# Kernel tuning notes

Hardware: AMD Instinct MI355X
Metric: run time of the kernel (lower is better)

Reference implementation:

```python
import jax, jax.numpy as jnp
import numpy as np

N, D, DFF, E, K = 2048, 1024, 4096, 8, 2  # tokens, d_model, d_ff, num_expert, top_k


def setup_inputs() -> dict:
    key = jax.random.key(0)
    ks = jax.random.split(key, 5)
    s = 0.02  # init scale
    return {
        "moe_inp": jax.random.normal(ks[0], (N, D), jnp.float32),
        "Wg": jax.random.normal(ks[1], (D, E), jnp.float32) * s,   # gate linear
        "bg": jnp.zeros((E,), jnp.float32),
        "W1": jax.random.normal(ks[2], (E, D, DFF), jnp.float32) * s,  # htoh4 per expert
        "b1": jnp.zeros((E, DFF), jnp.float32),
        "W2": jax.random.normal(ks[3], (E, DFF, D), jnp.float32) * s,  # h4toh per expert
        "b2": jnp.zeros((E, D), jnp.float32),
    }


def reference(moe_inp, Wg, bg, W1, b1, W2, b2):
    # --- NaiveGate: top-k experts per token, softmax over selected logits ---
    logits = moe_inp @ Wg + bg                      # [N, E]
    top_val, top_idx = jax.lax.top_k(logits, K)     # [N, K]
    score = jax.nn.softmax(top_val, axis=-1)        # [N, K]

    # Dense combine weights c[n, e] = sum_j score[n, j] * 1{top_idx[n, j] == e}.
    # This is the mathematically exact equivalent of scatter -> grouped expert
    # GEMM -> gather -> score-weighted combine in fmoe.
    comb = jnp.einsum(
        "nke,nk->ne", jax.nn.one_hot(top_idx, E, dtype=moe_inp.dtype), score
    )                                               # [N, E]

    # --- per-expert FFN: relu(x W1 + b1) W2 + b2, masked-combined by comb ---
    h = jax.nn.relu(jnp.einsum("nd,edh->enh", moe_inp, W1) + b1[:, None, :])  # [E, N, DFF]
    out = jnp.einsum("enh,ehd,ne->nd", h, W2, comb) + comb @ b2               # [N, D]
    return out
```

## Files before the change

### kernel.cpp

```cpp
#include <hip/hip_runtime.h>
#include <hip/hip_bf16.h>
#include <cstdint>
#include <cstddef>

#define NTOKS  2048
#define DMODEL 1024
#define DFFN   4096
#define NEXP   8
#define TS256  24
#define TS128  40

typedef __attribute__((ext_vector_type(8))) short short8;
typedef __attribute__((ext_vector_type(4))) float f32x4;
typedef __attribute__((ext_vector_type(4))) unsigned short u16x4;
typedef __attribute__((ext_vector_type(8))) unsigned short u16x8;

static constexpr size_t alignup(size_t x) { return (x + 255) & ~(size_t)255; }
static constexpr size_t OFF_XB   = 0;
static constexpr size_t OFF_CNT  = alignup(OFF_XB + (size_t)(NTOKS + 1) * DMODEL * 2);
static constexpr size_t OFF_OFFS = OFF_CNT + 256;
static constexpr size_t OFF_TOKE = OFF_OFFS + 256;
static constexpr size_t OFF_TOKT = OFF_TOKE + (size_t)NTOKS * 2 * 4;
static constexpr size_t OFF_TOKS = OFF_TOKT + (size_t)NTOKS * 2 * 4;
static constexpr size_t OFF_TI   = alignup(OFF_TOKS + (size_t)NTOKS * 2 * 4);
static constexpr size_t OFF_TI2  = OFF_TI + 256;
static constexpr size_t OFF_CAP  = alignup(OFF_TI2 + TS128 * 8);
static constexpr size_t OFF_H    = alignup(OFF_CAP + (size_t)NEXP * NTOKS * 4);
static constexpr size_t OFF_Y    = alignup(OFF_H + (size_t)(NTOKS * 2 + 256) * DFFN * 2);
static constexpr size_t OFF_WB   = alignup(OFF_Y + (size_t)2 * NTOKS * 2 * DMODEL * 4);

__device__ inline unsigned short f2bf(float f) {
  __hip_bfloat16 h = __float2bfloat16(f);
  return __builtin_bit_cast(unsigned short, h);
}

__device__ inline void gload16(const void* g, void* l) {
  __builtin_amdgcn_global_load_lds((const __attribute__((address_space(1))) unsigned int*)g,
                                   (__attribute__((address_space(3))) unsigned int*)l, 16, 0, 0);
}

__global__ __launch_bounds__(256) void k_convert(const float* __restrict__ x,
                                                 unsigned short* __restrict__ xb,
                                                 int* __restrict__ cnt) {
  if (blockIdx.x == 0 && threadIdx.x < NEXP) cnt[threadIdx.x] = 0;
  size_t base = ((size_t)blockIdx.x * 256 + threadIdx.x) * 8;
  const size_t total = (size_t)(NTOKS + 1) * DMODEL;
  if (base >= total) return;
  u16x8 o;
  if (base < (size_t)NTOKS * DMODEL) {
    f32x4 a = *(const f32x4*)(x + base);
    f32x4 b = *(const f32x4*)(x + base + 4);
#pragma unroll
    for (int j = 0; j < 4; ++j) { o[j] = f2bf(a[j]); o[4 + j] = f2bf(b[j]); }
  } else {
#pragma unroll
    for (int j = 0; j < 8; ++j) o[j] = 0;
  }
  *(u16x8*)(xb + base) = o;
}

template <int R, int C>
__global__ __launch_bounds__(256) void k_transconv(const float* __restrict__ W,
                                                   unsigned short* __restrict__ WT) {
  __shared__ unsigned short T[64][66];
  const int e = blockIdx.z;
  const int c0 = blockIdx.x * 64, r0 = blockIdx.y * 64;
  const float* Wp = W + (size_t)e * R * C;
  unsigned short* Tp = WT + (size_t)e * R * C;
  const int tid = threadIdx.x;
  const int rr = tid >> 4, cc = (tid & 15) << 2;
#pragma unroll
  for (int i = 0; i < 4; ++i) {
    int r = rr + (i << 4);
    f32x4 v = *(const f32x4*)(Wp + (size_t)(r0 + r) * C + c0 + cc);
    T[r][cc]     = f2bf(v[0]);
    T[r][cc + 1] = f2bf(v[1]);
    T[r][cc + 2] = f2bf(v[2]);
    T[r][cc + 3] = f2bf(v[3]);
  }
  __syncthreads();
  const int c = tid >> 2, kc = (tid & 3) << 4;
  u16x8 o0, o1;
#pragma unroll
  for (int i = 0; i < 8; ++i) { o0[i] = T[kc + i][c]; o1[i] = T[kc + 8 + i][c]; }
  unsigned short* dst = Tp + (size_t)(c0 + c) * R + r0 + kc;
  *(u16x8*)(dst) = o0;
  *(u16x8*)(dst + 8) = o1;
}

__global__ __launch_bounds__(256) void k_gate(const float* __restrict__ x,
                                              const float* __restrict__ Wg,
                                              const float* __restrict__ bg,
                                              int* __restrict__ cnt,
                                              int* __restrict__ tok_e,
                                              int* __restrict__ tok_t,
                                              float* __restrict__ tok_s,
                                              int* __restrict__ cap) {
  const int w = threadIdx.x >> 6, lane = threadIdx.x & 63;
  const int n = blockIdx.x * 4 + w;
  float acc[8];
#pragma unroll
  for (int e = 0; e < 8; ++e) acc[e] = 0.f;
  const float* xr = x + (size_t)n * DMODEL;
#pragma unroll 4
  for (int it = 0; it < DMODEL / 64; ++it) {
    int d = it * 64 + lane;
    float xv = xr[d];
    f32x4 w0 = *(const f32x4*)(Wg + d * 8);
    f32x4 w1 = *(const f32x4*)(Wg + d * 8 + 4);
#pragma unroll
    for (int j = 0; j < 4; ++j) { acc[j] += xv * w0[j]; acc[4 + j] += xv * w1[j]; }
  }
#pragma unroll
  for (int e = 0; e < 8; ++e)
#pragma unroll
    for (int off = 32; off; off >>= 1) acc[e] += __shfl_xor(acc[e], off, 64);
  if (lane == 0) {
    float l[8];
#pragma unroll
    for (int e = 0; e < 8; ++e) l[e] = acc[e] + bg[e];
    int i0 = 0; float v0 = l[0];
#pragma unroll
    for (int e = 1; e < 8; ++e) if (l[e] > v0) { v0 = l[e]; i0 = e; }
    int i1 = (i0 == 0) ? 1 : 0; float v1 = l[i1];
#pragma unroll
    for (int e = 0; e < 8; ++e) if (e != i0 && l[e] > v1) { v1 = l[e]; i1 = e; }
    float t = expf(v1 - v0);
    float inv = 1.f / (1.f + t);
    float s0 = inv, s1 = t * inv;
    int t0 = atomicAdd(&cnt[i0], 1);
    int t1 = atomicAdd(&cnt[i1], 1);
    cap[i0 * NTOKS + t0] = n;
    cap[i1 * NTOKS + t1] = n;
    tok_e[2 * n] = i0; tok_e[2 * n + 1] = i1;
    tok_t[2 * n] = t0; tok_t[2 * n + 1] = t1;
    tok_s[2 * n] = s0; tok_s[2 * n + 1] = s1;
  }
}

__global__ void k_scan(const int* __restrict__ cnt, int* __restrict__ offs,
                       int2* __restrict__ ti256, int2* __restrict__ ti128) {
  if (threadIdx.x == 0) {
    int s = 0;
#pragma unroll
    for (int e = 0; e < NEXP; ++e) { offs[e] = s; s += cnt[e]; }
    int a = 0;
    for (int e = 0; e < NEXP; ++e)
      for (int t = 0; t * 256 < cnt[e]; ++t) { ti256[a] = make_int2(e, t * 256); ++a; }
    for (; a < TS256; ++a) ti256[a] = make_int2(-1, 0);
    int b = 0;
    for (int e = 0; e < NEXP; ++e)
      for (int t = 0; t * 128 < cnt[e]; ++t) { ti128[b] = make_int2(e, t * 128); ++b; }
    for (; b < TS128; ++b) ti128[b] = make_int2(-1, 0);
  }
}

__global__ __launch_bounds__(512, 2) void k_gemm8(const unsigned short* __restrict__ Asrc,
                                                  const unsigned short* __restrict__ Bsrc,
                                                  const float* __restrict__ bias,
                                                  const int* __restrict__ cnt,
                                                  const int* __restrict__ offs,
                                                  const int2* __restrict__ tinfo,
                                                  const int* __restrict__ cap,
                                                  unsigned short* __restrict__ hout) {
  constexpr int KTOT = DMODEL, NTOT = DFFN;
  constexpr int NTILES = KTOT / 64;
  constexpr int NI = NTILES / 2;
  const int2 ti = tinfo[blockIdx.y];
  if (ti.x < 0) return;
  const int e = ti.x, t0 = ti.y;
  const int c = cnt[e];
  const int base = offs[e] + t0;
  const int n0 = blockIdx.x * 256;

  const int tid = threadIdx.x, w = tid >> 6, lane = tid & 63;
  const int l15 = lane & 15, lq = lane >> 4;
  const int wr = w >> 2, wc = w & 3;

  __shared__ unsigned short As[2][256 * 64];
  __shared__ unsigned short Bs[2][256 * 64];

  const int rl = tid >> 3;
  const int sw = ((tid & 7) ^ (rl & 7)) << 3;
  const unsigned short* aptr[4];
#pragma unroll
  for (int r = 0; r < 4; ++r) {
    int row = r * 64 + rl;
    size_t gr = (size_t)((t0 + row < c) ? cap[e * NTOKS + t0 + row] : NTOKS);
    aptr[r] = Asrc + gr * (size_t)KTOT + sw;
  }
  const unsigned short* Be = Bsrc + (size_t)e * ((size_t)KTOT * NTOT);
  const unsigned short* bptr[4];
#pragma unroll
  for (int r = 0; r < 4; ++r)
    bptr[r] = Be + (size_t)(n0 + r * 64 + rl) * KTOT + sw;

  auto stage_tile = [&](int tl) {
    const int b = tl & 1;
    const int k0 = tl << 6;
#pragma unroll
    for (int r = 0; r < 4; ++r)
      gload16(aptr[r] + k0, &As[b][(r * 64 + (w << 3)) << 6]);
#pragma unroll
    for (int r = 0; r < 4; ++r)
      gload16(bptr[r] + k0, &Bs[b][(r * 64 + (w << 3)) << 6]);
  };

  f32x4 acc[8][4] = {};
  short8 alo[4], ahi[4];
  const int sw0 = (lq ^ (l15 & 7)) << 3;

  stage_tile(0);
  asm volatile("s_waitcnt vmcnt(0)" ::: "memory");
  __builtin_amdgcn_s_barrier();
  asm volatile("" ::: "memory");

#define PHASE(BUF, MH, NH)                                                          \
  {                                                                                 \
    if ((NH) == 0) {                                                                \
      _Pragma("unroll")                                                             \
      for (int mm = 0; mm < 4; ++mm) {                                              \
        const unsigned short* ab =                                                  \
            &As[BUF][((wr * 128 + (MH) * 64 + mm * 16 + l15) << 6)];                \
        alo[mm] = *(const short8*)&ab[sw0];                                         \
        ahi[mm] = *(const short8*)&ab[sw0 ^ 32];                                    \
      }                                                                             \
    }                                                                               \
    short8 blo[2], bhi[2];                                                          \
    _Pragma("unroll")                                                               \
    for (int nn = 0; nn < 2; ++nn) {                                                \
      const unsigned short* bb =                                                    \
          &Bs[BUF][((wc * 64 + (NH) * 32 + nn * 16 + l15) << 6)];                   \
      blo[nn] = *(const short8*)&bb[sw0];                                           \
      bhi[nn] = *(const short8*)&bb[sw0 ^ 32];                                      \
    }                                                                               \
    asm volatile("" ::: "memory");                                                  \
    __builtin_amdgcn_s_setprio(1);                                                  \
    _Pragma("unroll")                                                               \
    for (int mm = 0; mm < 4; ++mm)                                                  \
      _Pragma("unroll")                                                             \
      for (int nn = 0; nn < 2; ++nn) {                                              \
        acc[(MH) * 4 + mm][(NH) * 2 + nn] =                                         \
            __builtin_amdgcn_mfma_f32_16x16x32_bf16(                                \
                alo[mm], blo[nn], acc[(MH) * 4 + mm][(NH) * 2 + nn], 0, 0, 0);      \
        acc[(MH) * 4 + mm][(NH) * 2 + nn] =                                         \
            __builtin_amdgcn_mfma_f32_16x16x32_bf16(                                \
                ahi[mm], bhi[nn], acc[(MH) * 4 + mm][(NH) * 2 + nn], 0, 0, 0);      \
      }                                                                             \
    __builtin_amdgcn_s_setprio(0);                                                  \
  }
#define FENCE_BAR                                                                   \
  asm volatile("" ::: "memory");                                                    \
  __builtin_amdgcn_s_barrier();                                                     \
  asm volatile("" ::: "memory");
#define DRAIN_BAR                                                                   \
  asm volatile("s_waitcnt vmcnt(0)" ::: "memory");                                  \
  __builtin_amdgcn_s_barrier();                                                     \
  asm volatile("" ::: "memory");

  for (int i = 0; i < NI; ++i) {
    const int t2 = 2 * i;
    stage_tile(t2 + 1);
    PHASE(0, 0, 0) FENCE_BAR
    PHASE(0, 0, 1) FENCE_BAR
    PHASE(0, 1, 0) FENCE_BAR
    PHASE(0, 1, 1) DRAIN_BAR
    if (i + 1 < NI) stage_tile(t2 + 2);
    PHASE(1, 0, 0) FENCE_BAR
    PHASE(1, 0, 1) FENCE_BAR
    PHASE(1, 1, 0) FENCE_BAR
    PHASE(1, 1, 1) DRAIN_BAR
  }
#undef PHASE
#undef FENCE_BAR
#undef DRAIN_BAR

  const float* be = bias + (size_t)e * NTOT;
#pragma unroll
  for (int m = 0; m < 8; ++m) {
#pragma unroll
    for (int q2 = 0; q2 < 4; ++q2) {
      int row = wr * 128 + m * 16 + lq * 4 + q2;
      if (t0 + row < c) {
        unsigned short* hr = hout + (size_t)(base + row) * NTOT;
#pragma unroll
        for (int nn = 0; nn < 4; ++nn) {
          int col = n0 + wc * 64 + nn * 16 + l15;
          float v = acc[m][nn][q2] + be[col];
          v = v > 0.f ? v : 0.f;
          hr[col] = f2bf(v);
        }
      }
    }
  }
}

template <int KTOT, int NTOT, int BN, bool FIRST, int KSPLIT>
__global__ __launch_bounds__(256) void k_gemm(const unsigned short* __restrict__ Asrc,
                                              const unsigned short* __restrict__ Bsrc,
                                              const float* __restrict__ bias,
                                              const int* __restrict__ cnt,
                                              const int* __restrict__ offs,
                                              const int2* __restrict__ tinfo,
                                              const int* __restrict__ cap,
                                              unsigned short* __restrict__ hout,
                                              float* __restrict__ yout) {
  const int2 ti = tinfo[blockIdx.y];
  if (ti.x < 0) return;
  const int e = ti.x, t0 = ti.y;
  const int c = cnt[e];
  const int base = offs[e] + t0;
  const int n0 = blockIdx.x * BN;
  constexpr int KCH = KTOT / KSPLIT;
  constexpr int NT = KCH / 32;
  const int kb = blockIdx.z * KCH;

  const int tid = threadIdx.x, w = tid >> 6, lane = tid & 63;
  const int l15 = lane & 15, lq = lane >> 4;
  constexpr int MR = 4;
  constexpr int NR = BN / 32;
  constexpr int BR = BN / 64;
  const int wr = w >> 1, wc = w & 1;

  __shared__ unsigned short As[2][128 * 32];
  __shared__ unsigned short Bs[2][BN * 32];

  const int rl = tid >> 2;
  const int sw = (((tid & 3) ^ (rl & 3) ^ ((rl >> 2) & 3)) << 3);
  const unsigned short* aptr[2];
#pragma unroll
  for (int r = 0; r < 2; ++r) {
    int row = r * 64 + rl;
    size_t gr;
    if constexpr (FIRST) gr = (size_t)((t0 + row < c) ? cap[e * NTOKS + t0 + row] : NTOKS);
    else                 gr = (size_t)(base + row);
    aptr[r] = Asrc + gr * (size_t)KTOT + kb + sw;
  }
  const unsigned short* Be = Bsrc + (size_t)e * ((size_t)KTOT * NTOT);
  const unsigned short* bptr[BR];
#pragma unroll
  for (int r = 0; r < BR; ++r)
    bptr[r] = Be + (size_t)(n0 + r * 64 + rl) * KTOT + kb + sw;

  auto stageA = [&](int k0, int b) {
#pragma unroll
    for (int r = 0; r < 2; ++r)
      gload16(aptr[r] + k0, &As[b][(r * 64 + w * 16) << 5]);
  };
  auto stageB = [&](int k0, int b) {
#pragma unroll
    for (int r = 0; r < BR; ++r)
      gload16(bptr[r] + k0, &Bs[b][(r * 64 + w * 16) << 5]);
  };

  f32x4 acc[MR][NR] = {};

  stageA(0, 0);
  stageB(0, 0);
  __syncthreads();

  int buf = 0;
  for (int t = 0; t < NT; ++t) {
    const int nxt = buf ^ 1;
    if (t + 1 < NT) { stageA((t + 1) * 32, nxt); stageB((t + 1) * 32, nxt); }

    short8 a[MR], b[NR];
    const int sw0 = ((lq ^ (l15 & 3) ^ ((l15 >> 2) & 3)) << 3);
#pragma unroll
    for (int m = 0; m < MR; ++m)
      a[m] = *(const short8*)&As[buf][((wr * 64 + m * 16 + l15) << 5) + sw0];
#pragma unroll
    for (int nn = 0; nn < NR; ++nn)
      b[nn] = *(const short8*)&Bs[buf][((wc * (BN / 2) + nn * 16 + l15) << 5) + sw0];
#pragma unroll
    for (int m = 0; m < MR; ++m)
#pragma unroll
      for (int nn = 0; nn < NR; ++nn)
        acc[m][nn] = __builtin_amdgcn_mfma_f32_16x16x32_bf16(a[m], b[nn], acc[m][nn], 0, 0, 0);

    __syncthreads();
    buf = nxt;
  }

  if constexpr (FIRST) {
    const float* be = bias + (size_t)e * NTOT;
#pragma unroll
    for (int m = 0; m < MR; ++m) {
#pragma unroll
      for (int q2 = 0; q2 < 4; ++q2) {
        int row = wr * 64 + m * 16 + lq * 4 + q2;
        if (t0 + row < c) {
          unsigned short* hr = hout + (size_t)(base + row) * NTOT;
#pragma unroll
          for (int nn = 0; nn < NR; ++nn) {
            int col = n0 + wc * (BN / 2) + nn * 16 + l15;
            float v = acc[m][nn][q2] + be[col];
            v = v > 0.f ? v : 0.f;
            hr[col] = f2bf(v);
          }
        }
      }
    }
  } else {
    float* yz = yout + (size_t)blockIdx.z * NTOKS * 2 * DMODEL;
#pragma unroll
    for (int m = 0; m < MR; ++m) {
#pragma unroll
      for (int q2 = 0; q2 < 4; ++q2) {
        int row = wr * 64 + m * 16 + lq * 4 + q2;
        if (t0 + row < c) {
          float* yr = yz + (size_t)(base + row) * NTOT;
#pragma unroll
          for (int nn = 0; nn < NR; ++nn) {
            int col = n0 + wc * (BN / 2) + nn * 16 + l15;
            yr[col] = acc[m][nn][q2];
          }
        }
      }
    }
  }
}

__global__ __launch_bounds__(256) void k_combine(const float* __restrict__ y,
                                                 const float* __restrict__ b2,
                                                 const int* __restrict__ tok_e,
                                                 const int* __restrict__ tok_t,
                                                 const float* __restrict__ tok_s,
                                                 const int* __restrict__ offs,
                                                 float* __restrict__ out) {
  const int n = blockIdx.x, t = threadIdx.x;
  const float* y1 = y + (size_t)NTOKS * 2 * DMODEL;
  const int e0 = tok_e[2 * n], e1 = tok_e[2 * n + 1];
  const int s0i = offs[e0] + tok_t[2 * n];
  const int s1i = offs[e1] + tok_t[2 * n + 1];
  const float sc0 = tok_s[2 * n], sc1 = tok_s[2 * n + 1];
  f32x4 v0 = *(const f32x4*)(y + (size_t)s0i * DMODEL + t * 4);
  f32x4 u0 = *(const f32x4*)(y1 + (size_t)s0i * DMODEL + t * 4);
  f32x4 v1 = *(const f32x4*)(y + (size_t)s1i * DMODEL + t * 4);
  f32x4 u1 = *(const f32x4*)(y1 + (size_t)s1i * DMODEL + t * 4);
  f32x4 c0 = *(const f32x4*)(b2 + (size_t)e0 * DMODEL + t * 4);
  f32x4 c1 = *(const f32x4*)(b2 + (size_t)e1 * DMODEL + t * 4);
  f32x4 r = sc0 * ((v0 + u0) + c0) + sc1 * ((v1 + u1) + c1);
  *(f32x4*)(out + (size_t)n * DMODEL + t * 4) = r;
}

extern "C" void kernel_launch(void* const* d_in, const int* in_sizes, int n_in,
                              void* d_out, int out_size, void* d_ws, size_t ws_size,
                              hipStream_t stream) {
  const float* x  = (const float*)d_in[0];
  const float* Wg = (const float*)d_in[1];
  const float* bg = (const float*)d_in[2];
  const float* W1 = (const float*)d_in[3];
  const float* b1 = (const float*)d_in[4];
  const float* W2 = (const float*)d_in[5];
  const float* b2 = (const float*)d_in[6];
  float* out = (float*)d_out;

  char* ws = (char*)d_ws;
  unsigned short* xb = (unsigned short*)(ws + OFF_XB);
  int*   cnt   = (int*)(ws + OFF_CNT);
  int*   offs  = (int*)(ws + OFF_OFFS);
  int*   tok_e = (int*)(ws + OFF_TOKE);
  int*   tok_t = (int*)(ws + OFF_TOKT);
  float* tok_s = (float*)(ws + OFF_TOKS);
  int2*  ti256 = (int2*)(ws + OFF_TI);
  int2*  ti128 = (int2*)(ws + OFF_TI2);
  int*   cap   = (int*)(ws + OFF_CAP);
  unsigned short* h  = (unsigned short*)(ws + OFF_H);
  float* y = (float*)(ws + OFF_Y);
  unsigned short* wb = (unsigned short*)(ws + OFF_WB);

  const int convBlocks = (int)(((size_t)(NTOKS + 1) * DMODEL / 8 + 255) / 256);
  k_convert<<<convBlocks, 256, 0, stream>>>(x, xb, cnt);
  k_gate<<<NTOKS / 4, 256, 0, stream>>>(x, Wg, bg, cnt, tok_e, tok_t, tok_s, cap);
  k_scan<<<1, 64, 0, stream>>>(cnt, offs, ti256, ti128);

  k_transconv<DMODEL, DFFN><<<dim3(DFFN / 64, DMODEL / 64, NEXP), 256, 0, stream>>>(W1, wb);
  k_gemm8<<<dim3(DFFN / 256, TS256), 512, 0, stream>>>(
      xb, wb, b1, cnt, offs, ti256, cap, h);

  k_transconv<DFFN, DMODEL><<<dim3(DMODEL / 64, DFFN / 64, NEXP), 256, 0, stream>>>(W2, wb);
  k_gemm<DFFN, DMODEL, 64, false, 2><<<dim3(DMODEL / 64, TS128, 2), 256, 0, stream>>>(
      h, wb, nullptr, cnt, offs, ti128, cap, nullptr, y);

  k_combine<<<NTOKS, 256, 0, stream>>>(y, b2, tok_e, tok_t, tok_s, offs, out);
}
```

Baseline: 291.2 us.

## Split tile staging into half-tiles interleaved with MFMA phases using partial vmcnt waits

Replaces the whole-tile prefetch plus full vmcnt(0) drain with four half-tile loads (A and B, each split in two), each issued between compute phases and guarded by vmcnt(6) barriers. The warp-to-tile mapping in LDS reads and in the epilogue is changed so each phase reads only the half that has already landed. Each freed half of the other buffer can then be refilled while the remaining phases run. The goal is finer-grained overlap of global-to-LDS traffic with MFMA work, which removes the full drain every tile. The cost is one redundant wrapped load on the last iteration and more barriers per tile.

```diff
diff --git a/kernel.cpp b/kernel.cpp
--- a/kernel.cpp
+++ b/kernel.cpp
@@ -164,8 +164,7 @@
                                                   const int* __restrict__ cap,
                                                   unsigned short* __restrict__ hout) {
   constexpr int KTOT = DMODEL, NTOT = DFFN;
-  constexpr int NTILES = KTOT / 64;
-  constexpr int NI = NTILES / 2;
+  constexpr int NT = KTOT / 64;
   const int2 ti = tinfo[blockIdx.y];
   if (ti.x < 0) return;
   const int e = ti.x, t0 = ti.y;
@@ -195,24 +194,41 @@
   for (int r = 0; r < 4; ++r)
     bptr[r] = Be + (size_t)(n0 + r * 64 + rl) * KTOT + sw;
 
-  auto stage_tile = [&](int tl) {
+  auto stageAh = [&](int tl, int h) {
     const int b = tl & 1;
-    const int k0 = tl << 6;
-#pragma unroll
-    for (int r = 0; r < 4; ++r)
-      gload16(aptr[r] + k0, &As[b][(r * 64 + (w << 3)) << 6]);
-#pragma unroll
-    for (int r = 0; r < 4; ++r)
-      gload16(bptr[r] + k0, &Bs[b][(r * 64 + (w << 3)) << 6]);
+    const int k0 = (tl % NT) << 6;
+#pragma unroll
+    for (int r = 0; r < 2; ++r) {
+      const int rg = h * 2 + r;
+      gload16(aptr[rg] + k0, &As[b][(rg * 64 + (w << 3)) << 6]);
+    }
+  };
+  auto stageBh = [&](int tl, int h) {
+    const int b = tl & 1;
+    const int k0 = (tl % NT) << 6;
+#pragma unroll
+    for (int r = 0; r < 2; ++r) {
+      const int rg = h * 2 + r;
+      gload16(bptr[rg] + k0, &Bs[b][(rg * 64 + (w << 3)) << 6]);
+    }
   };
 
   f32x4 acc[8][4] = {};
   short8 alo[4], ahi[4];
   const int sw0 = (lq ^ (l15 & 7)) << 3;
 
-  stage_tile(0);
-  asm volatile("s_waitcnt vmcnt(0)" ::: "memory");
-  __builtin_amdgcn_s_barrier();
+  stageAh(0, 0);
+  stageBh(0, 0);
+  stageBh(0, 1);
+  stageAh(0, 1);
+
+#define VM6_BAR                                                                     \
+  asm volatile("s_waitcnt vmcnt(6)" ::: "memory");                                  \
+  __builtin_amdgcn_s_barrier();                                                     \
+  asm volatile("" ::: "memory");
+#define BAR_ONLY                                                                    \
+  asm volatile("" ::: "memory");                                                    \
+  __builtin_amdgcn_s_barrier();                                                     \
   asm volatile("" ::: "memory");
 
 #define PHASE(BUF, MH, NH)                                                          \
@@ -221,7 +237,7 @@
       _Pragma("unroll")                                                             \
       for (int mm = 0; mm < 4; ++mm) {                                              \
         const unsigned short* ab =                                                  \
-            &As[BUF][((wr * 128 + (MH) * 64 + mm * 16 + l15) << 6)];                \
+            &As[BUF][(((MH) * 128 + wr * 64 + mm * 16 + l15) << 6)];                \
         alo[mm] = *(const short8*)&ab[sw0];                                         \
         ahi[mm] = *(const short8*)&ab[sw0 ^ 32];                                    \
       }                                                                             \
@@ -230,7 +246,7 @@
     _Pragma("unroll")                                                               \
     for (int nn = 0; nn < 2; ++nn) {                                                \
       const unsigned short* bb =                                                    \
-          &Bs[BUF][((wc * 64 + (NH) * 32 + nn * 16 + l15) << 6)];                   \
+          &Bs[BUF][(((NH) * 128 + wc * 32 + nn * 16 + l15) << 6)];                  \
       blo[nn] = *(const short8*)&bb[sw0];                                           \
       bhi[nn] = *(const short8*)&bb[sw0 ^ 32];                                      \
     }                                                                               \
@@ -249,43 +265,37 @@
       }                                                                             \
     __builtin_amdgcn_s_setprio(0);                                                  \
   }
-#define FENCE_BAR                                                                   \
-  asm volatile("" ::: "memory");                                                    \
-  __builtin_amdgcn_s_barrier();                                                     \
-  asm volatile("" ::: "memory");
-#define DRAIN_BAR                                                                   \
-  asm volatile("s_waitcnt vmcnt(0)" ::: "memory");                                  \
-  __builtin_amdgcn_s_barrier();                                                     \
-  asm volatile("" ::: "memory");
-
-  for (int i = 0; i < NI; ++i) {
-    const int t2 = 2 * i;
-    stage_tile(t2 + 1);
-    PHASE(0, 0, 0) FENCE_BAR
-    PHASE(0, 0, 1) FENCE_BAR
-    PHASE(0, 1, 0) FENCE_BAR
-    PHASE(0, 1, 1) DRAIN_BAR
-    if (i + 1 < NI) stage_tile(t2 + 2);
-    PHASE(1, 0, 0) FENCE_BAR
-    PHASE(1, 0, 1) FENCE_BAR
-    PHASE(1, 1, 0) FENCE_BAR
-    PHASE(1, 1, 1) DRAIN_BAR
+
+  for (int t = 0; t < NT; ++t) {
+    const int cur = t & 1;
+    stageAh(t + 1, 0);
+    VM6_BAR
+    PHASE(cur, 0, 0)
+    stageBh(t + 1, 0);
+    VM6_BAR
+    PHASE(cur, 0, 1)
+    stageBh(t + 1, 1);
+    VM6_BAR
+    PHASE(cur, 1, 0)
+    stageAh(t + 1, 1);
+    BAR_ONLY
+    PHASE(cur, 1, 1)
   }
 #undef PHASE
-#undef FENCE_BAR
-#undef DRAIN_BAR
+#undef VM6_BAR
+#undef BAR_ONLY
 
   const float* be = bias + (size_t)e * NTOT;
 #pragma unroll
   for (int m = 0; m < 8; ++m) {
 #pragma unroll
     for (int q2 = 0; q2 < 4; ++q2) {
-      int row = wr * 128 + m * 16 + lq * 4 + q2;
+      int row = (m >> 2) * 128 + wr * 64 + (m & 3) * 16 + lq * 4 + q2;
       if (t0 + row < c) {
         unsigned short* hr = hout + (size_t)(base + row) * NTOT;
 #pragma unroll
         for (int nn = 0; nn < 4; ++nn) {
-          int col = n0 + wc * 64 + nn * 16 + l15;
+          int col = n0 + (nn >> 1) * 128 + wc * 32 + (nn & 1) * 16 + l15;
           float v = acc[m][nn][q2] + be[col];
           v = v > 0.f ? v : 0.f;
           hr[col] = f2bf(v);
```

Result: no change. 293.8 us (+0.9%).
